# Kernel optimization log

Measured on AMD Instinct MI355X. Metric: run time of the kernel, lower is better.

Reference implementation:

```python
import jax, jax.numpy as jnp
import numpy as np

N, E, D, H = 50000, 640000, 128, 8
DK = D // H
EPS = 1e-5


def setup_inputs() -> dict:
    key = jax.random.key(0)
    ks = jax.random.split(key, 12)
    return {
        "x": jax.random.normal(ks[0], (N, D), dtype=jnp.float32),
        "edge_index": jax.random.randint(ks[1], (2, E), 0, N, dtype=jnp.int64),
        "edge_weight": jax.random.uniform(ks[2], (E,), dtype=jnp.float32),
        "x_time": jax.random.uniform(ks[3], (N,), dtype=jnp.float32),
        "edge_time": jax.random.uniform(ks[4], (E,), dtype=jnp.float32),
        "Wk": jax.random.normal(ks[5], (H, D, DK), dtype=jnp.float32) * 0.05,
        "bk": jnp.zeros((H, DK), dtype=jnp.float32),
        "Wq": jax.random.normal(ks[6], (H, D, DK), dtype=jnp.float32) * 0.05,
        "bq": jnp.zeros((H, DK), dtype=jnp.float32),
        "Wv": jax.random.normal(ks[7], (H, D, DK), dtype=jnp.float32) * 0.05,
        "bv": jnp.zeros((H, DK), dtype=jnp.float32),
    }


def _temporal_encoding(t):
    # t: [E] scalar times -> [E, D] sinusoidal encoding (TemporalEncoding)
    j = np.arange(D)
    div_term = (1.0 / np.power(10000.0, 2.0 * (j // 2) / D)).astype(np.float32)
    pos = (t * 200.0)[:, None] * div_term  # [E, D]
    even = jnp.asarray(j % 2 == 0)
    return jnp.where(even, jnp.sin(pos), jnp.cos(pos))


def _layer_norm(x):
    mu = jnp.mean(x, axis=-1, keepdims=True)
    var = jnp.mean(jnp.square(x - mu), axis=-1, keepdims=True)
    return (x - mu) * jax.lax.rsqrt(var + EPS)


def reference(x, edge_index, edge_weight, x_time, edge_time, Wk, bk, Wq, bq, Wv, bv):
    num_nodes = x_time.shape[0]
    src = edge_index[0]  # j (sender)
    dst = edge_index[1]  # i (receiver), also edge_index_i

    residual = x
    xn = _layer_norm(x)

    # asymmetric normalization: deg over edge_index[0]
    deg = jax.ops.segment_sum(edge_weight, src, num_segments=num_nodes)
    deg_inv = jnp.where(deg > 0, 1.0 / deg, 0.0)
    ew = deg_inv[src] * edge_weight  # [E]

    x_j = xn[src]                       # [E, D]
    x_i = xn[dst]                       # [E, D]
    x_j_t = x_j + _temporal_encoding(edge_time)  # [E, D]

    k = jnp.einsum("ed,hdk->ehk", x_j_t, Wk) + bk  # [E, H, DK]
    q = jnp.einsum("ed,hdk->ehk", x_i, Wq) + bq    # [E, H, DK]
    v = jnp.einsum("ed,hdk->ehk", x_j_t, Wv) + bv  # [E, H, DK]

    attn = jnp.sum(k * q, axis=-1) / np.sqrt(DK)   # [E, H]
    attn = attn * ew[:, None]

    # scatter softmax over receiver neighborhoods, per head
    m = jax.ops.segment_max(attn, dst, num_segments=num_nodes)   # [N, H]
    ex = jnp.exp(attn - m[dst])                                  # [E, H]
    den = jax.ops.segment_sum(ex, dst, num_segments=num_nodes)   # [N, H]
    attn_norm = ex / den[dst]                                    # [E, H]

    msg = (attn_norm[:, :, None] * v).reshape(-1, H * DK)        # [E, D]
    aggr = jax.ops.segment_sum(msg, dst, num_segments=num_nodes)  # [N, D]

    return residual + jax.nn.gelu(aggr, approximate=False)
```

## Files before the change

### kernel.cpp

```cpp
#include <hip/hip_runtime.h>
#include <hip/hip_bf16.h>

constexpr int D_ = 128;
constexpr int DK_ = 16;
constexpr int TBL = 4096;

typedef __attribute__((ext_vector_type(8))) short short8;
typedef __attribute__((ext_vector_type(4))) float f32x4;
typedef unsigned char uchar;

__device__ __forceinline__ ushort f2b(float f) {
    uint b = __float_as_uint(f);
    uint r = (b + 0x7fffu + ((b >> 16) & 1u)) >> 16;
    return (ushort)r;
}
__device__ __forceinline__ uchar q8(float v) {
    float t = fmaf(v, 31.75f, 128.5f);
    t = fminf(fmaxf(t, 0.0f), 255.0f);
    return (uchar)(uint)t;
}
__device__ __forceinline__ float fexp2(float x) {
#if __has_builtin(__builtin_amdgcn_exp2f)
    return __builtin_amdgcn_exp2f(x);
#else
    return exp2f(x);
#endif
}
__device__ __forceinline__ float frcp(float x) {
#if __has_builtin(__builtin_amdgcn_rcpf)
    return __builtin_amdgcn_rcpf(x);
#else
    return 1.0f / x;
#endif
}

__global__ __launch_bounds__(256)
void k_front(const float2* __restrict__ x2, uint* __restrict__ xnb,
             const float* __restrict__ Wk, const float* __restrict__ Wv,
             uchar* __restrict__ gkv,
             const float* __restrict__ Wq, const float* __restrict__ bq,
             const float* __restrict__ bk, const float* __restrict__ bv,
             ushort* __restrict__ WTb, float* __restrict__ BB,
             const int* __restrict__ ei, const float* __restrict__ ewt,
             const float* __restrict__ etime,
             int* __restrict__ cnt, float* __restrict__ deg, uint2* __restrict__ pp2,
             int N, int E, int RPB) {
    __shared__ float te[16][128];
    __shared__ int sor;
    int b = blockIdx.x;
    int tid = threadIdx.x;
    int wv = tid >> 6, lane = tid & 63;

    int2 det = ((const int2*)ei)[tid];
    if (tid == 0) sor = 0;
    __syncthreads();
    atomicOr(&sor, det.y);
    __syncthreads();
    int e = b * 256 + tid;
    bool act = (e < E);
    int s = 0, dd = 0, rank = 0;
    float t = 0.f;
    if (act) {
        if (sor == 0) { s = ((const int2*)ei)[e].x; dd = ((const int2*)ei)[E + e].x; }
        else          { s = ei[e];                  dd = ei[E + e]; }
        t = etime[e];
        atomicAdd(&deg[s], ewt[e]);
        rank = atomicAdd(&cnt[dd], 1);
    }

    if (b < TBL / 16) {
        int t0 = b * 16;
        int j = tid & 127, half = tid >> 7;
        float freq = 200.0f * exp2f(-(float)(j >> 1) * (13.287712379549449f / 64.0f));
        bool isCos = (j & 1);
        #pragma unroll
        for (int bb = 0; bb < 8; ++bb) {
            float tt = (float)(t0 + half * 8 + bb) * (1.0f / (float)(TBL - 1));
            float arg = tt * freq;
            te[half * 8 + bb][j] = isCos ? cosf(arg) : sinf(arg);
        }
        __syncthreads();
        int h = j >> 4, kk = j & 15;
        float ak[8] = {}, av[8] = {};
        for (int d = 0; d < 128; ++d) {
            float wk = Wk[(h * 128 + d) * 16 + kk];
            float wvv = Wv[(h * 128 + d) * 16 + kk];
            float tvs[8];
            #pragma unroll
            for (int bb = 0; bb < 8; ++bb) tvs[bb] = te[half * 8 + bb][d];
            #pragma unroll
            for (int bb = 0; bb < 8; ++bb) { ak[bb] += tvs[bb] * wk; av[bb] += tvs[bb] * wvv; }
        }
        int off = ((j >> 2) << 3) + (j & 3);
        #pragma unroll
        for (int bb = 0; bb < 8; ++bb) {
            size_t row = (size_t)(t0 + half * 8 + bb);
            gkv[row * 256 + off]     = q8(ak[bb]);
            gkv[row * 256 + off + 4] = q8(av[bb]);
        }
    } else if (b < TBL / 16 + 192) {
        int i = (b - TBL / 16) * 256 + tid;
        int c = i >> 7, d = i & 127;
        int m = c >> 7, cl = c & 127;
        int h = cl >> 4, kk = cl & 15;
        const float* W = (m == 0) ? Wq : ((m == 1) ? Wk : Wv);
        WTb[i] = f2b(W[(h * D_ + d) * DK_ + kk]);
        if (i < 384) {
            int m2 = i >> 7, cl2 = i & 127;
            const float* bb = (m2 == 0) ? bq : ((m2 == 1) ? bk : bv);
            BB[i] = bb[cl2];
        }
    } else {
        int lnb = b - (TBL / 16 + 192);
        for (int i = 0;; ++i) {
            int rl = i * 4 + wv;
            if (rl >= RPB) break;
            int row = lnb * RPB + rl;
            if (row >= N) break;
            float2 v = x2[(size_t)row * 64 + lane];
            float sm = v.x + v.y;
            #pragma unroll
            for (int o = 1; o < 64; o <<= 1) sm += __shfl_xor(sm, o);
            float mu = sm * (1.0f / 128.0f);
            float dx = v.x - mu, dy = v.y - mu;
            float s2 = dx * dx + dy * dy;
            #pragma unroll
            for (int o = 1; o < 64; o <<= 1) s2 += __shfl_xor(s2, o);
            float rs = rsqrtf(s2 * (1.0f / 128.0f) + 1e-5f);
            uint lo = f2b(dx * rs), hi = f2b(dy * rs);
            xnb[(size_t)row * 64 + lane] = (hi << 16) | lo;
        }
    }

    if (act) {
        int ti = (int)(t * (float)(TBL - 1) + 0.5f);
        ti = ti < 0 ? 0 : (ti > TBL - 1 ? TBL - 1 : ti);
        uint2 r;
        r.x = (uint)s | ((uint)dd << 16);
        r.y = (uint)rank | ((uint)ti << 16);
        pp2[e] = r;
    }
}

__global__ __launch_bounds__(256)
void k_gemm(const ushort* __restrict__ xnb, const ushort* __restrict__ WTb,
            const float* __restrict__ BB,
            uchar* __restrict__ qnb, uchar* __restrict__ kvb, int N) {
    __shared__ short As[128 * 128];
    __shared__ short Bs[128 * 128];
    int tid = threadIdx.x;
    int rowBlk = blockIdx.x, cb = blockIdx.y;

    short8 av[8], bv[8];
    int chunk = tid & 15;
    #pragma unroll
    for (int i = 0; i < 8; ++i) {
        int row = i * 16 + (tid >> 4);
        int gRow = rowBlk * 128 + row;
        if (gRow < N) av[i] = *(const short8*)(xnb + (size_t)gRow * 128 + chunk * 8);
        else          av[i] = short8{0, 0, 0, 0, 0, 0, 0, 0};
        int gCol = cb * 128 + row;
        bv[i] = *(const short8*)(WTb + (size_t)gCol * 128 + chunk * 8);
    }
    #pragma unroll
    for (int i = 0; i < 8; ++i) {
        int row = i * 16 + (tid >> 4);
        int widx = row * 128 + ((chunk * 8) ^ ((row & 7) * 8));
        *(short8*)&As[widx] = av[i];
        *(short8*)&Bs[widx] = bv[i];
    }
    __syncthreads();

    int wv = tid >> 6, lane = tid & 63;
    int wr = wv >> 1, wc = wv & 1;
    int l15 = lane & 15, g = lane >> 4;

    f32x4 acc[4][4];
    #pragma unroll
    for (int m = 0; m < 4; ++m)
        #pragma unroll
        for (int n = 0; n < 4; ++n) acc[m][n] = f32x4{0.f, 0.f, 0.f, 0.f};

    #pragma unroll
    for (int kt = 0; kt < 4; ++kt) {
        int kshort = kt * 32 + g * 8;
        short8 af[4], bf[4];
        #pragma unroll
        for (int m = 0; m < 4; ++m) {
            int r = wr * 64 + m * 16 + l15;
            af[m] = *(const short8*)&As[r * 128 + (kshort ^ ((r & 7) * 8))];
        }
        #pragma unroll
        for (int n = 0; n < 4; ++n) {
            int c = wc * 64 + n * 16 + l15;
            bf[n] = *(const short8*)&Bs[c * 128 + (kshort ^ ((c & 7) * 8))];
        }
        #pragma unroll
        for (int m = 0; m < 4; ++m)
            #pragma unroll
            for (int n = 0; n < 4; ++n)
                acc[m][n] = __builtin_amdgcn_mfma_f32_16x16x32_bf16(af[m], bf[n], acc[m][n], 0, 0, 0);
    }

    float bb[4];
    #pragma unroll
    for (int n = 0; n < 4; ++n) bb[n] = BB[cb * 128 + wc * 64 + n * 16 + l15];

    #pragma unroll
    for (int m = 0; m < 4; ++m) {
        int R0 = rowBlk * 128 + wr * 64 + m * 16 + g * 4;
        #pragma unroll
        for (int n = 0; n < 4; ++n) {
            int cl = wc * 64 + n * 16 + l15;
            #pragma unroll
            for (int r = 0; r < 4; ++r) {
                int row = R0 + r;
                if (row >= N) continue;
                float val = acc[m][n][r] + bb[n];
                if (cb == 0) {
                    qnb[(size_t)row * 128 + cl] = q8(val);
                } else {
                    int off = ((cl >> 2) << 3) + (cl & 3) + ((cb == 2) ? 4 : 0);
                    kvb[(size_t)row * 256 + off] = q8(val);
                }
            }
        }
    }
}

__global__ __launch_bounds__(256)
void k_scanA(const int* __restrict__ cnt, int* __restrict__ csum) {
    __shared__ int sh[256];
    int b = blockIdx.x, t = threadIdx.x;
    int base = b * 1024 + t * 4;
    int s = cnt[base] + cnt[base + 1] + cnt[base + 2] + cnt[base + 3];
    sh[t] = s;
    __syncthreads();
    for (int off = 128; off > 0; off >>= 1) {
        if (t < off) sh[t] += sh[t + off];
        __syncthreads();
    }
    if (t == 0) csum[b] = sh[0];
}

__global__ void k_scanB(int* __restrict__ csum, int nch) {
    if (blockIdx.x == 0 && threadIdx.x == 0) {
        int run = 0;
        for (int i = 0; i < nch; ++i) { int v = csum[i]; csum[i] = run; run += v; }
    }
}

__global__ __launch_bounds__(256)
void k_scanC(const int* __restrict__ cnt, const int* __restrict__ csum,
             int* __restrict__ rowptr) {
    __shared__ int sh[256];
    int b = blockIdx.x, t = threadIdx.x;
    int base = b * 1024 + t * 4;
    int v0 = cnt[base], v1 = cnt[base + 1], v2 = cnt[base + 2], v3 = cnt[base + 3];
    int tot = v0 + v1 + v2 + v3;
    sh[t] = tot;
    __syncthreads();
    for (int off = 1; off < 256; off <<= 1) {
        int add = (t >= off) ? sh[t - off] : 0;
        __syncthreads();
        sh[t] += add;
        __syncthreads();
    }
    int excl = sh[t] - tot + csum[b];
    rowptr[base]     = excl;
    rowptr[base + 1] = excl + v0;
    rowptr[base + 2] = excl + v0 + v1;
    rowptr[base + 3] = excl + v0 + v1 + v2;
}

__global__ __launch_bounds__(256)
void k_scatter(const uint2* __restrict__ pp2, const float* __restrict__ ewt,
               const float* __restrict__ deg, const int* __restrict__ rowptr,
               uint2* __restrict__ erec, int E) {
    const float C = 0.25f * 1.4426950408889634f / 1008.0625f;
    int e = blockIdx.x * 256 + threadIdx.x;
    if (e >= E) return;
    uint2 P = pp2[e];
    int s = (int)(P.x & 0xffffu), dd = (int)(P.x >> 16);
    int rank = (int)(P.y & 0xffffu);
    uint ti = P.y >> 16;
    float dg = deg[s];
    float ewc = dg > 0.f ? ewt[e] * C / dg : 0.f;
    int pos = rowptr[dd] + rank;
    uint2 r;
    r.x = (uint)s | (ti << 16);
    r.y = __float_as_uint(ewc);
    erec[pos] = r;
}

#define AGGR_BODY(JJ, MASKED)                                                               \
    {                                                                                       \
        uint2 r = erec[(JJ) + ((MASKED) ? 0 : half)];                                       \
        int s = (int)(r.x & 0xffffu), ti = (int)(r.x >> 16);                                 \
        uint2 kv = *(const uint2*)(kvb + (size_t)s * 256 + 8 * c);                          \
        uint2 gg = *(const uint2*)(gkv + (size_t)ti * 256 + 8 * c);                         \
        float p = -Q256;                                                                    \
        p = fmaf((float)(kv.x & 0xffu)         + (float)(gg.x & 0xffu),         qf0, p);    \
        p = fmaf((float)((kv.x >> 8) & 0xffu)  + (float)((gg.x >> 8) & 0xffu),  qf1, p);    \
        p = fmaf((float)((kv.x >> 16) & 0xffu) + (float)((gg.x >> 16) & 0xffu), qf2, p);    \
        p = fmaf((float)(kv.x >> 24)           + (float)(gg.x >> 24),           qf3, p);    \
        p += __shfl_xor(p, 1);                                                              \
        p += __shfl_xor(p, 2);                                                              \
        float ex = fexp2(p * __uint_as_float(r.y));                                         \
        if (MASKED && half) ex = 0.f;                                                       \
        den += ex;                                                                          \
        n0 = fmaf(ex, (float)(kv.y & 0xffu)         + (float)(gg.y & 0xffu),         n0);   \
        n1 = fmaf(ex, (float)((kv.y >> 8) & 0xffu)  + (float)((gg.y >> 8) & 0xffu),  n1);   \
        n2 = fmaf(ex, (float)((kv.y >> 16) & 0xffu) + (float)((gg.y >> 16) & 0xffu), n2);   \
        n3 = fmaf(ex, (float)(kv.y >> 24)           + (float)(gg.y >> 24),           n3);   \
    }

__global__ __launch_bounds__(256)
void k_aggr(const int* __restrict__ rowptr, const uint2* __restrict__ erec,
            const uchar* __restrict__ qnb, const uchar* __restrict__ kvb,
            const uchar* __restrict__ gkv,
            const float4* __restrict__ x4, float4* __restrict__ out4, int N) {
    int w = (int)((blockIdx.x * (size_t)blockDim.x + threadIdx.x) >> 6);
    if (w >= N) return;
    int lane = threadIdx.x & 63;
    int c = lane & 31;
    int half = lane >> 5;

    uint qv = *(const uint*)(qnb + (size_t)w * 128 + 4 * c);
    float qf0 = (float)(qv & 0xffu) - 128.0f;
    float qf1 = (float)((qv >> 8) & 0xffu) - 128.0f;
    float qf2 = (float)((qv >> 16) & 0xffu) - 128.0f;
    float qf3 = (float)(qv >> 24) - 128.0f;
    float Q256 = 256.0f * (qf0 + qf1 + qf2 + qf3);

    float n0 = 0.f, n1 = 0.f, n2 = 0.f, n3 = 0.f, den = 0.f;
    int beg = rowptr[w], end = rowptr[w + 1];

    int j = beg;
    for (; j + 4 <= end; j += 4) {
        AGGR_BODY(j, 0)
        AGGR_BODY(j + 2, 0)
    }
    for (; j + 2 <= end; j += 2) AGGR_BODY(j, 0)
    if (j < end) AGGR_BODY(j, 1)

    den += __shfl_xor(den, 32);
    n0 += __shfl_xor(n0, 32);
    n1 += __shfl_xor(n1, 32);
    n2 += __shfl_xor(n2, 32);
    n3 += __shfl_xor(n3, 32);

    if (half == 0) {
        const float S = 1.0f / 31.75f;
        float inv  = den > 0.f ? frcp(den) : 0.f;
        float c256 = den > 0.f ? 256.f : 0.f;
        float a0 = S * (n0 * inv - c256);
        float a1 = S * (n1 * inv - c256);
        float a2 = S * (n2 * inv - c256);
        float a3 = S * (n3 * inv - c256);
        float4 xx = x4[(size_t)w * 32 + c];
        float4 o;
        o.x = xx.x + 0.5f * a0 * (1.0f + erff(a0 * 0.70710678118f));
        o.y = xx.y + 0.5f * a1 * (1.0f + erff(a1 * 0.70710678118f));
        o.z = xx.z + 0.5f * a2 * (1.0f + erff(a2 * 0.70710678118f));
        o.w = xx.w + 0.5f * a3 * (1.0f + erff(a3 * 0.70710678118f));
        out4[(size_t)w * 32 + c] = o;
    }
}

extern "C" void kernel_launch(void* const* d_in, const int* in_sizes, int n_in,
                              void* d_out, int out_size, void* d_ws, size_t ws_size,
                              hipStream_t stream) {
    const float* x    = (const float*)d_in[0];
    const int*   ei   = (const int*)d_in[1];
    const float* ewt  = (const float*)d_in[2];
    const float* etim = (const float*)d_in[4];
    const float* Wk   = (const float*)d_in[5];
    const float* bk   = (const float*)d_in[6];
    const float* Wq   = (const float*)d_in[7];
    const float* bq   = (const float*)d_in[8];
    const float* Wv   = (const float*)d_in[9];
    const float* bv   = (const float*)d_in[10];
    int N = in_sizes[3];
    int E = in_sizes[2];
    float* out = (float*)d_out;

    int NCH = (N + 1 + 1023) / 1024;
    int NP = NCH * 1024;

    char* base = (char*)d_ws;
    size_t off = 0;
    auto alloc = [&](size_t bytes) {
        char* r = base + off;
        off += (bytes + 255) & ~size_t(255);
        return r;
    };
    ushort* xnb = (ushort*)alloc((size_t)N * 128 * 2);
    uchar*  qnb = (uchar*)alloc((size_t)N * 128);
    uchar*  kvb = (uchar*)alloc((size_t)N * 256);
    uchar*  gkv = (uchar*)alloc((size_t)TBL * 256);
    ushort* WTb = (ushort*)alloc(384 * 128 * 2);
    float*  BB  = (float*)alloc(384 * 4);
    float*  deg = (float*)alloc((size_t)N * 4);
    uint2*  pp2 = (uint2*)alloc((size_t)E * 8);
    int*    cnt    = (int*)alloc((size_t)NP * 4);
    int*    rowptr = (int*)alloc((size_t)NP * 4);
    int*    csum   = (int*)alloc((size_t)NCH * 4);
    uint2*  erec   = (uint2*)xnb;

    hipMemsetAsync(cnt, 0, (size_t)NP * sizeof(int), stream);
    hipMemsetAsync(deg, 0, (size_t)N * sizeof(float), stream);

    int EB = (E + 255) / 256;
    int FIX = TBL / 16 + 192;
    int blocks = EB > FIX + 1 ? EB : FIX + 1;
    int lnBlocks = blocks - FIX;
    int RPB = (N + lnBlocks - 1) / lnBlocks;
    k_front<<<blocks, 256, 0, stream>>>((const float2*)x, (uint*)xnb,
                                        Wk, Wv, gkv, Wq, bq, bk, bv, WTb, BB,
                                        ei, ewt, etim, cnt, deg, pp2,
                                        N, E, RPB);

    dim3 ggrid((N + 127) / 128, 3);
    k_gemm<<<ggrid, 256, 0, stream>>>(xnb, WTb, BB, qnb, kvb, N);

    k_scanA<<<NCH, 256, 0, stream>>>(cnt, csum);
    k_scanB<<<1, 64, 0, stream>>>(csum, NCH);
    k_scanC<<<NCH, 256, 0, stream>>>(cnt, csum, rowptr);

    k_scatter<<<(E + 255) / 256, 256, 0, stream>>>(pp2, ewt, deg, rowptr, erec, E);

    int agrid = (int)(((size_t)N * 64 + 255) / 256);
    k_aggr<<<agrid, 256, 0, stream>>>(rowptr, erec, qnb, kvb, gkv,
                                      (const float4*)x, (float4*)out, N);
}
```

Baseline: 176.7 us.

## Process two edges per thread, fold scan carry into scanC, unroll aggregation

The front kernel now handles two edges per thread, which halves the grid and changes how many blocks do layer-norm rows (RPB). The serial single-thread scanB kernel is removed, and each scanC block instead sums the preceding chunk totals with a wave reduction, saving one launch. The aggregation loop is unrolled to eight edges per iteration for more memory-level parallelism. Risks: the wave prefix covers at most 64 chunks, and fewer front blocks mean less parallelism for the layer-norm part.

```diff
diff --git a/kernel.cpp b/kernel.cpp
--- a/kernel.cpp
+++ b/kernel.cpp
@@ -56,26 +56,30 @@
     __syncthreads();
     atomicOr(&sor, det.y);
     __syncthreads();
-    int e = b * 256 + tid;
-    bool act = (e < E);
-    int s = 0, dd = 0, rank = 0;
-    float t = 0.f;
-    if (act) {
-        if (sor == 0) { s = ((const int2*)ei)[e].x; dd = ((const int2*)ei)[E + e].x; }
-        else          { s = ei[e];                  dd = ei[E + e]; }
-        t = etime[e];
-        atomicAdd(&deg[s], ewt[e]);
-        rank = atomicAdd(&cnt[dd], 1);
-    }
+    int e0 = b * 512 + tid, e1 = e0 + 256;
+    bool a0 = (e0 < E), a1 = (e1 < E);
+    int s0 = 0, d0 = 0, r0 = 0, s1 = 0, d1 = 0, r1 = 0;
+    float t0 = 0.f, t1 = 0.f;
+    if (sor == 0) {
+        if (a0) { s0 = ((const int2*)ei)[e0].x; d0 = ((const int2*)ei)[E + e0].x; }
+        if (a1) { s1 = ((const int2*)ei)[e1].x; d1 = ((const int2*)ei)[E + e1].x; }
+    } else {
+        if (a0) { s0 = ei[e0]; d0 = ei[E + e0]; }
+        if (a1) { s1 = ei[e1]; d1 = ei[E + e1]; }
+    }
+    if (a0) { t0 = etime[e0]; atomicAdd(&deg[s0], ewt[e0]); }
+    if (a1) { t1 = etime[e1]; atomicAdd(&deg[s1], ewt[e1]); }
+    if (a0) r0 = atomicAdd(&cnt[d0], 1);
+    if (a1) r1 = atomicAdd(&cnt[d1], 1);
 
     if (b < TBL / 16) {
-        int t0 = b * 16;
+        int tb0 = b * 16;
         int j = tid & 127, half = tid >> 7;
         float freq = 200.0f * exp2f(-(float)(j >> 1) * (13.287712379549449f / 64.0f));
         bool isCos = (j & 1);
         #pragma unroll
         for (int bb = 0; bb < 8; ++bb) {
-            float tt = (float)(t0 + half * 8 + bb) * (1.0f / (float)(TBL - 1));
+            float tt = (float)(tb0 + half * 8 + bb) * (1.0f / (float)(TBL - 1));
             float arg = tt * freq;
             te[half * 8 + bb][j] = isCos ? cosf(arg) : sinf(arg);
         }
@@ -94,7 +98,7 @@
         int off = ((j >> 2) << 3) + (j & 3);
         #pragma unroll
         for (int bb = 0; bb < 8; ++bb) {
-            size_t row = (size_t)(t0 + half * 8 + bb);
+            size_t row = (size_t)(tb0 + half * 8 + bb);
             gkv[row * 256 + off]     = q8(ak[bb]);
             gkv[row * 256 + off + 4] = q8(av[bb]);
         }
@@ -132,13 +136,21 @@
         }
     }
 
-    if (act) {
-        int ti = (int)(t * (float)(TBL - 1) + 0.5f);
+    if (a0) {
+        int ti = (int)(t0 * (float)(TBL - 1) + 0.5f);
         ti = ti < 0 ? 0 : (ti > TBL - 1 ? TBL - 1 : ti);
         uint2 r;
-        r.x = (uint)s | ((uint)dd << 16);
-        r.y = (uint)rank | ((uint)ti << 16);
-        pp2[e] = r;
+        r.x = (uint)s0 | ((uint)d0 << 16);
+        r.y = (uint)r0 | ((uint)ti << 16);
+        pp2[e0] = r;
+    }
+    if (a1) {
+        int ti = (int)(t1 * (float)(TBL - 1) + 0.5f);
+        ti = ti < 0 ? 0 : (ti > TBL - 1 ? TBL - 1 : ti);
+        uint2 r;
+        r.x = (uint)s1 | ((uint)d1 << 16);
+        r.y = (uint)r1 | ((uint)ti << 16);
+        pp2[e1] = r;
     }
 }
 
@@ -243,18 +255,18 @@
     if (t == 0) csum[b] = sh[0];
 }
 
-__global__ void k_scanB(int* __restrict__ csum, int nch) {
-    if (blockIdx.x == 0 && threadIdx.x == 0) {
-        int run = 0;
-        for (int i = 0; i < nch; ++i) { int v = csum[i]; csum[i] = run; run += v; }
-    }
-}
-
 __global__ __launch_bounds__(256)
 void k_scanC(const int* __restrict__ cnt, const int* __restrict__ csum,
-             int* __restrict__ rowptr) {
+             int* __restrict__ rowptr, int nch) {
     __shared__ int sh[256];
+    __shared__ int sExcl;
     int b = blockIdx.x, t = threadIdx.x;
+    if (t < 64) {
+        int v = (t < b && t < nch) ? csum[t] : 0;
+        #pragma unroll
+        for (int o = 1; o < 64; o <<= 1) v += __shfl_xor(v, o);
+        if (t == 0) sExcl = v;
+    }
     int base = b * 1024 + t * 4;
     int v0 = cnt[base], v1 = cnt[base + 1], v2 = cnt[base + 2], v3 = cnt[base + 3];
     int tot = v0 + v1 + v2 + v3;
@@ -266,7 +278,7 @@
         sh[t] += add;
         __syncthreads();
     }
-    int excl = sh[t] - tot + csum[b];
+    int excl = sh[t] - tot + sExcl;
     rowptr[base]     = excl;
     rowptr[base + 1] = excl + v0;
     rowptr[base + 2] = excl + v0 + v1;
@@ -337,9 +349,11 @@
     int beg = rowptr[w], end = rowptr[w + 1];
 
     int j = beg;
-    for (; j + 4 <= end; j += 4) {
+    for (; j + 8 <= end; j += 8) {
         AGGR_BODY(j, 0)
         AGGR_BODY(j + 2, 0)
+        AGGR_BODY(j + 4, 0)
+        AGGR_BODY(j + 6, 0)
     }
     for (; j + 2 <= end; j += 2) AGGR_BODY(j, 0)
     if (j < end) AGGR_BODY(j, 1)
@@ -411,7 +425,7 @@
     hipMemsetAsync(cnt, 0, (size_t)NP * sizeof(int), stream);
     hipMemsetAsync(deg, 0, (size_t)N * sizeof(float), stream);
 
-    int EB = (E + 255) / 256;
+    int EB = (E + 511) / 512;
     int FIX = TBL / 16 + 192;
     int blocks = EB > FIX + 1 ? EB : FIX + 1;
     int lnBlocks = blocks - FIX;
@@ -425,8 +439,7 @@
     k_gemm<<<ggrid, 256, 0, stream>>>(xnb, WTb, BB, qnb, kvb, N);
 
     k_scanA<<<NCH, 256, 0, stream>>>(cnt, csum);
-    k_scanB<<<1, 64, 0, stream>>>(csum, NCH);
-    k_scanC<<<NCH, 256, 0, stream>>>(cnt, csum, rowptr);
+    k_scanC<<<NCH, 256, 0, stream>>>(cnt, csum, rowptr, NCH);
 
     k_scatter<<<(E + 255) / 256, 256, 0, stream>>>(pp2, ewt, deg, rowptr, erec, E);
 
```

Result: slower. 183.5 us (+3.9%).
